# Kernel tuning notes

Hardware: AMD Instinct MI355X
Metric: run time of the kernel (lower is better)

The kernel has to match this reference:

```python
import jax, jax.numpy as jnp
import numpy as np


def setup_inputs() -> dict:
    key = jax.random.key(0)
    kq, kk, kv, km = jax.random.split(key, 4)
    B, H, S, D = 1, 16, 2048, 64
    q = jax.random.normal(kq, (B, H, S, D), dtype=jnp.float32)
    k = jax.random.normal(kk, (B, H, S, D), dtype=jnp.float32)
    v = jax.random.normal(kv, (B, H, S, D), dtype=jnp.float32)
    # Boolean attention mask: True = attend, False = ignore.
    # block-pruned use case while keeping the same dense-mask semantics.
    BLK = 64
    tile = jax.random.bernoulli(km, 0.5, (B, H, S // BLK, S // BLK))
    mask = jnp.repeat(jnp.repeat(tile, BLK, axis=2), BLK, axis=3)
    # Guarantee at least something per row is allowed in most rows is not
    # required: fully-masked rows legitimately produce zero output.
    return {"q": q, "k": k, "v": v, "mask": mask}


def reference(q, k, v, mask):
    # Masked scaled-dot-product attention; rows with no valid keys output 0,
    # matching the kernel's `acc / l_i if l_i > 0 else 0` behavior.
    D = q.shape[-1]
    scale = 1.0 / jnp.sqrt(jnp.asarray(D, q.dtype))
    qk = jnp.einsum("bhqd,bhkd->bhqk", q, k) * scale          # [B,H,S,S]
    neg_inf = jnp.asarray(-jnp.inf, qk.dtype)
    s = jnp.where(mask, qk, neg_inf)
    m = jnp.max(s, axis=-1, keepdims=True)                      # row max (may be -inf)
    m_safe = jnp.where(jnp.isfinite(m), m, jnp.zeros_like(m))
    p = jnp.where(mask, jnp.exp(s - m_safe), jnp.zeros_like(qk))  # unnormalized probs
    l = jnp.sum(p, axis=-1, keepdims=True)                      # [B,H,S,1]
    acc = jnp.einsum("bhqk,bhkd->bhqd", p, v)
    out = jnp.where(l > 0, acc / jnp.where(l > 0, l, jnp.ones_like(l)), jnp.zeros_like(acc))
    return out
```

## Files before the change

kernel.cpp:

```cpp
#include <hip/hip_runtime.h>
#include <hip/hip_bf16.h>
#include <stdint.h>

typedef __bf16 bf16;
typedef __attribute__((ext_vector_type(4))) __bf16 bf16x4;
typedef __attribute__((ext_vector_type(8))) __bf16 bf16x8;
typedef __attribute__((ext_vector_type(4))) float f32x4;
typedef __attribute__((ext_vector_type(4))) unsigned int u32x4;

#define NH 16
#define SEQ 2048
#define DH 64
#define NT 32
#define SCALE 0.125f
#define NEGINF (-1e30f)
#define IMG_TILE 8192

#define WS_KIMG  65536
#define WS_VIMG  (WS_KIMG + (size_t)NH * NT * IMG_TILE)
#define WS_NEED  (WS_VIMG + (size_t)NH * NT * IMG_TILE)

__device__ __forceinline__ unsigned swz16(int row, int bytecol) {
  return (unsigned)(row * 128 + (bytecol ^ ((row & 7) << 4)));
}

__global__ void __launch_bounds__(256) conv_kernel(
    const float* __restrict__ kg, const float* __restrict__ vg,
    unsigned char* __restrict__ ws)
{
  const int b = blockIdx.x, tid = threadIdx.x;
  const int h = b & 15, kt = (b >> 4) & 31, which = b >> 9;
  const int kb = kt << 6;
  __shared__ float T[64][65];
  const int row = tid >> 2, c0 = (tid & 3) * 16;

  const float* src = which ? vg : kg;
  {
    const f32x4* rp = (const f32x4*)(src + ((size_t)(h * SEQ) + kb + row) * DH + c0);
    f32x4 a0 = rp[0], a1 = rp[1], a2 = rp[2], a3 = rp[3];
    float* d = &T[row][c0];
    #pragma unroll
    for (int j = 0; j < 4; ++j) {
      d[j] = a0[j]; d[4 + j] = a1[j]; d[8 + j] = a2[j]; d[12 + j] = a3[j];
    }
  }
  __syncthreads();
  if (which == 0) {
    unsigned char* kimg = ws + WS_KIMG + (size_t)(h * NT + kt) * IMG_TILE;
    #pragma unroll
    for (int i = 0; i < 2; ++i) {
      const int slot = tid + 256 * i, g = slot >> 6, ll = slot & 63;
      const int nd = g >> 1, ks = g & 1;
      const float* s = &T[16 * nd + (ll & 15)][ks * 32 + (ll >> 4) * 8];
      bf16x8 o;
      #pragma unroll
      for (int j = 0; j < 8; ++j) o[j] = (bf16)s[j];
      *(bf16x8*)(kimg + slot * 16) = o;
    }
  } else {
    unsigned char* vimg = ws + WS_VIMG + (size_t)(h * NT + kt) * IMG_TILE;
    #pragma unroll
    for (int i = 0; i < 2; ++i) {
      const int slot = tid + 256 * i, g = slot >> 6, ll = slot & 63;
      const int nd = g >> 1, ks = g & 1;
      const int r0 = ks * 32 + (ll >> 4) * 8, col = 16 * nd + (ll & 15);
      bf16x8 o;
      #pragma unroll
      for (int j = 0; j < 8; ++j) o[j] = (bf16)T[r0 + j][col];
      *(bf16x8*)(vimg + slot * 16) = o;
    }
  }
}

template<bool IMG>
__global__ void __launch_bounds__(256, 4) fused_attn_kernel(
    const float* __restrict__ qg, const float* __restrict__ kg,
    const float* __restrict__ vg, const void* __restrict__ maskg,
    float* __restrict__ outg, const unsigned char* __restrict__ ws)
{
  const int bid = blockIdx.x;
  const int h = bid & 15, qt = bid >> 4, qb = qt << 6;
  const int tid = threadIdx.x, l = tid & 63, rw = tid >> 6;
  const int qrow = l & 15, kgrp = l >> 4;

  __shared__ __attribute__((aligned(16))) bf16 Pl[4][1024];
  __shared__ unsigned sOr[2][32], sAnd[2][32];
  __shared__ unsigned char tfl[32];
  __shared__ unsigned char Ll[32];
  __shared__ int lcnt;
  __shared__ int clsS;

  bf16x8 qa[2];
  {
    const float* qp = qg + ((size_t)(h * SEQ) + qb + 16 * rw + qrow) * DH;
    #pragma unroll
    for (int ks = 0; ks < 2; ++ks) {
      f32x4 x0 = *(const f32x4*)(qp + ks * 32 + kgrp * 8);
      f32x4 x1 = *(const f32x4*)(qp + ks * 32 + kgrp * 8 + 4);
      bf16x8 a;
      #pragma unroll
      for (int j = 0; j < 4; ++j) {
        a[j] = (bf16)(x0[j] * SCALE); a[4 + j] = (bf16)(x1[j] * SCALE);
      }
      qa[ks] = a;
    }
  }

  if (tid == 0) clsS = 0;
  __syncthreads();
  {
    u32x4 t = ((const u32x4*)maskg)[tid];
    int bits = 0;
    #pragma unroll
    for (int j = 0; j < 4; ++j) {
      if (t[j] == 0x01010101u) bits |= 1;
      else if (t[j] == 1u) bits |= 2;
    }
    const int wb = (__any(bits & 1) ? 1 : 0) | (__any(bits & 2) ? 2 : 0);
    if (l == 0 && wb) atomicOr(&clsS, wb);
  }
  __syncthreads();
  const int byteMode = ((clsS & 1) || !(clsS & 2)) ? 1 : 0;

  const int half = tid >> 7;
  if (byteMode) {
    const unsigned char* rp = (const unsigned char*)maskg
        + ((size_t)(h * SEQ) + qb + half * 63) * SEQ + (tid & 127) * 16;
    u32x4 t = *(const u32x4*)rp;
    unsigned o = t[0] | t[1] | t[2] | t[3];
    unsigned a = t[0] & t[1] & t[2] & t[3];
    o |= __shfl_xor(o, 1); a &= __shfl_xor(a, 1);
    o |= __shfl_xor(o, 2); a &= __shfl_xor(a, 2);
    if ((l & 3) == 0) {
      const int kt = ((tid >> 6) & 1) * 16 + (l >> 2);
      sOr[half][kt] = o; sAnd[half][kt] = a;
    }
  } else {
    const unsigned char* rbase = (const unsigned char*)maskg
        + ((size_t)(h * SEQ) + qb + half * 63) * (size_t)SEQ * 4;
    const int c0 = tid & 127;
    unsigned oo[4], aa[4];
    #pragma unroll
    for (int p = 0; p < 4; ++p) {
      u32x4 t = *(const u32x4*)(rbase + (p * 128 + c0) * 16);
      oo[p] = t[0] | t[1] | t[2] | t[3];
      aa[p] = t[0] & t[1] & t[2] & t[3];
    }
    #pragma unroll
    for (int d = 1; d <= 8; d <<= 1)
      #pragma unroll
      for (int p = 0; p < 4; ++p) {
        oo[p] |= __shfl_xor(oo[p], d); aa[p] &= __shfl_xor(aa[p], d);
      }
    if ((l & 15) == 0) {
      #pragma unroll
      for (int p = 0; p < 4; ++p) {
        const int kt = p * 8 + ((tid >> 6) & 1) * 4 + (l >> 4);
        sOr[half][kt] = oo[p]; sAnd[half][kt] = aa[p];
      }
    }
  }
  __syncthreads();
  if (tid < 32) {
    const int kt = tid;
    const unsigned o0 = sOr[0][kt], a0 = sAnd[0][kt];
    const unsigned o1 = sOr[1][kt], a1 = sAnd[1][kt];
    int active, allT = 0;
    if (o0 == a0 && o1 == a1 && o0 == o1) {
      if (o0 == 0u) active = 0;
      else {
        active = 1;
        allT = byteMode
             ? (((((a0 & 0x7F7F7F7Fu) + 0x7F7F7F7Fu) | a0) & 0x80808080u) == 0x80808080u)
             : 1;
      }
    } else {
      active = ((o0 | o1) != 0u);
    }
    tfl[kt] = (unsigned char)(active | (allT ? 2 : 0));
  }
  __syncthreads();
  if (tid == 0) {
    int n = 0;
    for (int kt = 0; kt < NT; ++kt) {
      const unsigned f = tfl[kt];
      if (f & 1) Ll[n++] = (unsigned char)(kt | ((f & 2) ? 0x80 : 0));
    }
    lcnt = n;
  }
  __syncthreads();
  const int cnt = lcnt;

  f32x4 oacc[4];
  #pragma unroll
  for (int nd = 0; nd < 4; ++nd) oacc[nd] = (f32x4){0.f, 0.f, 0.f, 0.f};
  float mrun = NEGINF, lrun = 0.f;

  auto loadK = [&](bf16x8 (&kf)[8], int kt) {
    if constexpr (IMG) {
      const unsigned char* kp = ws + WS_KIMG + (size_t)(h * NT + kt) * IMG_TILE + l * 16;
      #pragma unroll
      for (int g = 0; g < 8; ++g) kf[g] = *(const bf16x8*)(kp + g * 1024);
    } else {
      const int kb = kt << 6;
      #pragma unroll
      for (int g = 0; g < 8; ++g) {
        const int nd = g >> 1, ks = g & 1;
        const float* kr = kg + ((size_t)(h * SEQ) + kb + 16 * nd + qrow) * DH
                          + ks * 32 + kgrp * 8;
        f32x4 x0 = ((const f32x4*)kr)[0], x1 = ((const f32x4*)kr)[1];
        #pragma unroll
        for (int j = 0; j < 4; ++j) { kf[g][j] = (bf16)x0[j]; kf[g][4 + j] = (bf16)x1[j]; }
      }
    }
  };

  bf16x8 kf[8];
  if (cnt > 0) loadK(kf, Ll[0] & 63);

  char* pw = (char*)Pl[rw];

  for (int i = 0; i < cnt; ++i) {
    const unsigned e = Ll[i];
    const int kt = e & 63;
    const int allT = (e & 0x80u) != 0;
    const int kb = kt << 6;

    f32x4 sfr[4];
    #pragma unroll
    for (int nd = 0; nd < 4; ++nd) sfr[nd] = (f32x4){0.f, 0.f, 0.f, 0.f};
    __builtin_amdgcn_s_setprio(1);
    #pragma unroll
    for (int nd = 0; nd < 4; ++nd)
      #pragma unroll
      for (int ks = 0; ks < 2; ++ks)
        sfr[nd] = __builtin_amdgcn_mfma_f32_16x16x32_bf16(kf[nd * 2 + ks], qa[ks], sfr[nd], 0, 0, 0);
    __builtin_amdgcn_s_setprio(0);

    if (i + 1 < cnt) loadK(kf, Ll[i + 1] & 63);

    bf16x8 vf[8];
    if constexpr (IMG) {
      const unsigned char* vp = ws + WS_VIMG + (size_t)(h * NT + kt) * IMG_TILE + l * 16;
      #pragma unroll
      for (int g = 0; g < 8; ++g) vf[g] = *(const bf16x8*)(vp + g * 1024);
    } else {
      #pragma unroll
      for (int g = 0; g < 8; ++g) {
        const int nd = g >> 1, ks = g & 1;
        const float* vb = vg + ((size_t)(h * SEQ) + kb + ks * 32 + kgrp * 8) * DH
                          + 16 * nd + qrow;
        #pragma unroll
        for (int j = 0; j < 8; ++j) vf[g][j] = (bf16)vb[j * DH];
      }
    }

    if (!allT) {
      const size_t base = ((size_t)(h * SEQ) + qb + 16 * rw + qrow) * SEQ + kb + 4 * kgrp;
      #pragma unroll
      for (int nd = 0; nd < 4; ++nd)
        #pragma unroll
        for (int r = 0; r < 4; ++r) {
          const size_t off = base + 16 * nd + r;
          const bool mv = byteMode ? (((const unsigned char*)maskg)[off] != 0)
                                   : (((const unsigned*)maskg)[off] != 0u);
          if (!mv) sfr[nd][r] = NEGINF;
        }
    }

    float mt;
    {
      f32x4 t0, t1;
      #pragma unroll
      for (int r = 0; r < 4; ++r) {
        t0[r] = fmaxf(sfr[0][r], sfr[1][r]);
        t1[r] = fmaxf(sfr[2][r], sfr[3][r]);
      }
      mt = fmaxf(fmaxf(fmaxf(t0[0], t0[1]), fmaxf(t0[2], t0[3])),
                 fmaxf(fmaxf(t1[0], t1[1]), fmaxf(t1[2], t1[3])));
    }
    mt = fmaxf(mt, __shfl_xor(mt, 16));
    mt = fmaxf(mt, __shfl_xor(mt, 32));
    const float mn = fmaxf(mrun, mt);
    const float fac = __expf(mrun - mn);
    float ls = 0.f;
    bf16x4 pb[4];
    #pragma unroll
    for (int nd = 0; nd < 4; ++nd)
      #pragma unroll
      for (int r = 0; r < 4; ++r) {
        const float p = (sfr[nd][r] > -1e20f) ? __expf(sfr[nd][r] - mn) : 0.f;
        ls += p; pb[nd][r] = (bf16)p;
      }
    ls += __shfl_xor(ls, 16);
    ls += __shfl_xor(ls, 32);
    lrun = lrun * fac + ls;
    mrun = mn;
    #pragma unroll
    for (int nd = 0; nd < 4; ++nd)
      #pragma unroll
      for (int r = 0; r < 4; ++r) oacc[nd][r] *= fac;

    #pragma unroll
    for (int nd = 0; nd < 4; ++nd)
      *(bf16x4*)(pw + swz16(qrow, 32 * nd + 8 * kgrp)) = pb[nd];
    bf16x8 ap[2];
    #pragma unroll
    for (int ks = 0; ks < 2; ++ks)
      ap[ks] = *(const bf16x8*)(pw + swz16(qrow, 64 * ks + 16 * kgrp));

    __builtin_amdgcn_s_setprio(1);
    #pragma unroll
    for (int ks = 0; ks < 2; ++ks)
      #pragma unroll
      for (int nd = 0; nd < 4; ++nd)
        oacc[nd] = __builtin_amdgcn_mfma_f32_16x16x32_bf16(vf[nd * 2 + ks], ap[ks], oacc[nd], 0, 0, 0);
    __builtin_amdgcn_s_setprio(0);
  }

  {
    const float inv = (lrun > 0.f) ? (1.f / lrun) : 0.f;
    const int grow = qb + 16 * rw + qrow;
    float* op = outg + ((size_t)(h * SEQ) + grow) * DH + 4 * kgrp;
    #pragma unroll
    for (int nd = 0; nd < 4; ++nd) {
      f32x4 o;
      #pragma unroll
      for (int r = 0; r < 4; ++r) o[r] = oacc[nd][r] * inv;
      *(f32x4*)(op + 16 * nd) = o;
    }
  }
}

extern "C" void kernel_launch(void* const* d_in, const int* in_sizes, int n_in,
                              void* d_out, int out_size, void* d_ws, size_t ws_size,
                              hipStream_t stream) {
  const float* q = (const float*)d_in[0];
  const float* k = (const float*)d_in[1];
  const float* v = (const float*)d_in[2];
  const void*  m = d_in[3];
  float* out = (float*)d_out;
  unsigned char* ws = (unsigned char*)d_ws;

  if (ws_size >= WS_NEED) {
    conv_kernel<<<2 * NH * NT, 256, 0, stream>>>(k, v, ws);
    fused_attn_kernel<true><<<NH * NT, 256, 0, stream>>>(q, k, v, m, out, ws);
  } else {
    fused_attn_kernel<false><<<NH * NT, 256, 0, stream>>>(q, k, v, m, out, ws);
  }
}
```

Measured before the change: 40.10 us.

## Split key tiles across two wave groups per block and merge softmax state

Doubles the block to 512 threads so two groups of four waves each take alternate active key tiles for the same 64 query rows. At the end, the second group writes its running max, running sum and output accumulator to shared memory, and the first group rescales and combines both before writing the output. The aim is to halve the serial per-block loop over key tiles and raise the number of waves in flight per CU. The cost is more shared memory, an extra combine step with two block barriers, and higher register pressure under the new launch bounds.

```diff
diff --git a/kernel.cpp b/kernel.cpp
--- a/kernel.cpp
+++ b/kernel.cpp
@@ -73,17 +73,19 @@
 }
 
 template<bool IMG>
-__global__ void __launch_bounds__(256, 4) fused_attn_kernel(
+__global__ void __launch_bounds__(512, 4) fused_attn_kernel(
     const float* __restrict__ qg, const float* __restrict__ kg,
     const float* __restrict__ vg, const void* __restrict__ maskg,
     float* __restrict__ outg, const unsigned char* __restrict__ ws)
 {
   const int bid = blockIdx.x;
   const int h = bid & 15, qt = bid >> 4, qb = qt << 6;
-  const int tid = threadIdx.x, l = tid & 63, rw = tid >> 6;
+  const int tid = threadIdx.x, l = tid & 63, w = tid >> 6;
+  const int s = w >> 2, rw = w & 3;
   const int qrow = l & 15, kgrp = l >> 4;
 
-  __shared__ __attribute__((aligned(16))) bf16 Pl[4][1024];
+  __shared__ __attribute__((aligned(16))) bf16 Pl[8][1024];
+  __shared__ float mg[4][64][19];
   __shared__ unsigned sOr[2][32], sAnd[2][32];
   __shared__ unsigned char tfl[32];
   __shared__ unsigned char Ll[32];
@@ -122,41 +124,43 @@
   __syncthreads();
   const int byteMode = ((clsS & 1) || !(clsS & 2)) ? 1 : 0;
 
-  const int half = tid >> 7;
-  if (byteMode) {
-    const unsigned char* rp = (const unsigned char*)maskg
-        + ((size_t)(h * SEQ) + qb + half * 63) * SEQ + (tid & 127) * 16;
-    u32x4 t = *(const u32x4*)rp;
-    unsigned o = t[0] | t[1] | t[2] | t[3];
-    unsigned a = t[0] & t[1] & t[2] & t[3];
-    o |= __shfl_xor(o, 1); a &= __shfl_xor(a, 1);
-    o |= __shfl_xor(o, 2); a &= __shfl_xor(a, 2);
-    if ((l & 3) == 0) {
-      const int kt = ((tid >> 6) & 1) * 16 + (l >> 2);
-      sOr[half][kt] = o; sAnd[half][kt] = a;
-    }
-  } else {
-    const unsigned char* rbase = (const unsigned char*)maskg
-        + ((size_t)(h * SEQ) + qb + half * 63) * (size_t)SEQ * 4;
-    const int c0 = tid & 127;
-    unsigned oo[4], aa[4];
-    #pragma unroll
-    for (int p = 0; p < 4; ++p) {
-      u32x4 t = *(const u32x4*)(rbase + (p * 128 + c0) * 16);
-      oo[p] = t[0] | t[1] | t[2] | t[3];
-      aa[p] = t[0] & t[1] & t[2] & t[3];
-    }
-    #pragma unroll
-    for (int d = 1; d <= 8; d <<= 1)
+  if (tid < 256) {
+    const int half = tid >> 7;
+    if (byteMode) {
+      const unsigned char* rp = (const unsigned char*)maskg
+          + ((size_t)(h * SEQ) + qb + half * 63) * SEQ + (tid & 127) * 16;
+      u32x4 t = *(const u32x4*)rp;
+      unsigned o = t[0] | t[1] | t[2] | t[3];
+      unsigned a = t[0] & t[1] & t[2] & t[3];
+      o |= __shfl_xor(o, 1); a &= __shfl_xor(a, 1);
+      o |= __shfl_xor(o, 2); a &= __shfl_xor(a, 2);
+      if ((l & 3) == 0) {
+        const int kt = ((tid >> 6) & 1) * 16 + (l >> 2);
+        sOr[half][kt] = o; sAnd[half][kt] = a;
+      }
+    } else {
+      const unsigned char* rbase = (const unsigned char*)maskg
+          + ((size_t)(h * SEQ) + qb + half * 63) * (size_t)SEQ * 4;
+      const int c0 = tid & 127;
+      unsigned oo[4], aa[4];
       #pragma unroll
       for (int p = 0; p < 4; ++p) {
-        oo[p] |= __shfl_xor(oo[p], d); aa[p] &= __shfl_xor(aa[p], d);
-      }
-    if ((l & 15) == 0) {
-      #pragma unroll
-      for (int p = 0; p < 4; ++p) {
-        const int kt = p * 8 + ((tid >> 6) & 1) * 4 + (l >> 4);
-        sOr[half][kt] = oo[p]; sAnd[half][kt] = aa[p];
+        u32x4 t = *(const u32x4*)(rbase + (p * 128 + c0) * 16);
+        oo[p] = t[0] | t[1] | t[2] | t[3];
+        aa[p] = t[0] & t[1] & t[2] & t[3];
+      }
+      #pragma unroll
+      for (int d = 1; d <= 8; d <<= 1)
+        #pragma unroll
+        for (int p = 0; p < 4; ++p) {
+          oo[p] |= __shfl_xor(oo[p], d); aa[p] &= __shfl_xor(aa[p], d);
+        }
+      if ((l & 15) == 0) {
+        #pragma unroll
+        for (int p = 0; p < 4; ++p) {
+          const int kt = p * 8 + ((tid >> 6) & 1) * 4 + (l >> 4);
+          sOr[half][kt] = oo[p]; sAnd[half][kt] = aa[p];
+        }
       }
     }
   }
@@ -216,11 +220,11 @@
   };
 
   bf16x8 kf[8];
-  if (cnt > 0) loadK(kf, Ll[0] & 63);
-
-  char* pw = (char*)Pl[rw];
-
-  for (int i = 0; i < cnt; ++i) {
+  if (s < cnt) loadK(kf, Ll[s] & 63);
+
+  char* pw = (char*)Pl[w];
+
+  for (int i = s; i < cnt; i += 2) {
     const unsigned e = Ll[i];
     const int kt = e & 63;
     const int allT = (e & 0x80u) != 0;
@@ -237,7 +241,7 @@
         sfr[nd] = __builtin_amdgcn_mfma_f32_16x16x32_bf16(kf[nd * 2 + ks], qa[ks], sfr[nd], 0, 0, 0);
     __builtin_amdgcn_s_setprio(0);
 
-    if (i + 1 < cnt) loadK(kf, Ll[i + 1] & 63);
+    if (i + 2 < cnt) loadK(kf, Ll[i + 2] & 63);
 
     bf16x8 vf[8];
     if constexpr (IMG) {
@@ -318,15 +322,31 @@
     __builtin_amdgcn_s_setprio(0);
   }
 
-  {
-    const float inv = (lrun > 0.f) ? (1.f / lrun) : 0.f;
+  __syncthreads();
+  if (s == 1) {
+    float* mp = &mg[rw][l][0];
+    mp[0] = mrun; mp[1] = lrun;
+    #pragma unroll
+    for (int nd = 0; nd < 4; ++nd)
+      #pragma unroll
+      for (int r = 0; r < 4; ++r) mp[2 + nd * 4 + r] = oacc[nd][r];
+  }
+  __syncthreads();
+  if (s == 0) {
+    const float* mp = &mg[rw][l][0];
+    const float m1 = mp[0], l1 = mp[1];
+    const float ms = fmaxf(mrun, m1);
+    const float f0 = __expf(mrun - ms), f1 = __expf(m1 - ms);
+    const float li = lrun * f0 + l1 * f1;
+    const float inv = (li > 0.f) ? (1.f / li) : 0.f;
     const int grow = qb + 16 * rw + qrow;
     float* op = outg + ((size_t)(h * SEQ) + grow) * DH + 4 * kgrp;
     #pragma unroll
     for (int nd = 0; nd < 4; ++nd) {
       f32x4 o;
       #pragma unroll
-      for (int r = 0; r < 4; ++r) o[r] = oacc[nd][r] * inv;
+      for (int r = 0; r < 4; ++r)
+        o[r] = (oacc[nd][r] * f0 + mp[2 + nd * 4 + r] * f1) * inv;
       *(f32x4*)(op + 16 * nd) = o;
     }
   }
@@ -344,8 +364,8 @@
 
   if (ws_size >= WS_NEED) {
     conv_kernel<<<2 * NH * NT, 256, 0, stream>>>(k, v, ws);
-    fused_attn_kernel<true><<<NH * NT, 256, 0, stream>>>(q, k, v, m, out, ws);
+    fused_attn_kernel<true><<<NH * NT, 512, 0, stream>>>(q, k, v, m, out, ws);
   } else {
-    fused_attn_kernel<false><<<NH * NT, 256, 0, stream>>>(q, k, v, m, out, ws);
+    fused_attn_kernel<false><<<NH * NT, 512, 0, stream>>>(q, k, v, m, out, ws);
   }
 }
```

New measurement: 42.26 us. +5.4%, slower.

## Skip online-softmax rescale when max grows little and defer row-sum reduction

Applied to the files above, without the earlier changes.

Adds a lazy rescaling rule to the attention loop. The running max and the accumulator rescale are updated only when some lane's tile max exceeds the running max by more than 8, with the exponent threshold checked wave-wide. The per-tile cross-lane shuffles for the row sum are replaced by per-lane partial sums that are reduced once after the loop, and tiles with an all-true mask skip the -inf test on each element. The tile list entry is also made wave-uniform with readfirstlane. In exchange, probabilities can reach up to e^8 before normalization, which costs some precision headroom in bf16 and fp32, and the skip test adds a wave vote on each iteration.

```diff
diff --git a/kernel.cpp b/kernel.cpp
--- a/kernel.cpp
+++ b/kernel.cpp
@@ -194,7 +194,8 @@
   f32x4 oacc[4];
   #pragma unroll
   for (int nd = 0; nd < 4; ++nd) oacc[nd] = (f32x4){0.f, 0.f, 0.f, 0.f};
-  float mrun = NEGINF, lrun = 0.f;
+  float mrun = NEGINF;
+  float lrun = 0.f;
 
   auto loadK = [&](bf16x8 (&kf)[8], int kt) {
     if constexpr (IMG) {
@@ -216,14 +217,14 @@
   };
 
   bf16x8 kf[8];
-  if (cnt > 0) loadK(kf, Ll[0] & 63);
+  if (cnt > 0) loadK(kf, __builtin_amdgcn_readfirstlane((int)Ll[0]) & 63);
 
   char* pw = (char*)Pl[rw];
 
   for (int i = 0; i < cnt; ++i) {
-    const unsigned e = Ll[i];
+    const int e = __builtin_amdgcn_readfirstlane((int)Ll[i]);
     const int kt = e & 63;
-    const int allT = (e & 0x80u) != 0;
+    const int allT = (e & 0x80) != 0;
     const int kb = kt << 6;
 
     f32x4 sfr[4];
@@ -237,7 +238,7 @@
         sfr[nd] = __builtin_amdgcn_mfma_f32_16x16x32_bf16(kf[nd * 2 + ks], qa[ks], sfr[nd], 0, 0, 0);
     __builtin_amdgcn_s_setprio(0);
 
-    if (i + 1 < cnt) loadK(kf, Ll[i + 1] & 63);
+    if (i + 1 < cnt) loadK(kf, __builtin_amdgcn_readfirstlane((int)Ll[i + 1]) & 63);
 
     bf16x8 vf[8];
     if constexpr (IMG) {
@@ -268,7 +269,7 @@
         }
     }
 
-    float mt;
+    float pmax;
     {
       f32x4 t0, t1;
       #pragma unroll
@@ -276,30 +277,42 @@
         t0[r] = fmaxf(sfr[0][r], sfr[1][r]);
         t1[r] = fmaxf(sfr[2][r], sfr[3][r]);
       }
-      mt = fmaxf(fmaxf(fmaxf(t0[0], t0[1]), fmaxf(t0[2], t0[3])),
-                 fmaxf(fmaxf(t1[0], t1[1]), fmaxf(t1[2], t1[3])));
-    }
-    mt = fmaxf(mt, __shfl_xor(mt, 16));
-    mt = fmaxf(mt, __shfl_xor(mt, 32));
-    const float mn = fmaxf(mrun, mt);
-    const float fac = __expf(mrun - mn);
+      pmax = fmaxf(fmaxf(fmaxf(t0[0], t0[1]), fmaxf(t0[2], t0[3])),
+                   fmaxf(fmaxf(t1[0], t1[1]), fmaxf(t1[2], t1[3])));
+    }
+    if (!__all(pmax - mrun <= 8.f)) {
+      float mt = pmax;
+      mt = fmaxf(mt, __shfl_xor(mt, 16));
+      mt = fmaxf(mt, __shfl_xor(mt, 32));
+      const float mn = fmaxf(mrun, mt);
+      const float fac = __expf(mrun - mn);
+      lrun *= fac;
+      #pragma unroll
+      for (int nd = 0; nd < 4; ++nd)
+        #pragma unroll
+        for (int r = 0; r < 4; ++r) oacc[nd][r] *= fac;
+      mrun = mn;
+    }
     float ls = 0.f;
     bf16x4 pb[4];
-    #pragma unroll
-    for (int nd = 0; nd < 4; ++nd)
-      #pragma unroll
-      for (int r = 0; r < 4; ++r) {
-        const float p = (sfr[nd][r] > -1e20f) ? __expf(sfr[nd][r] - mn) : 0.f;
-        ls += p; pb[nd][r] = (bf16)p;
-      }
-    ls += __shfl_xor(ls, 16);
-    ls += __shfl_xor(ls, 32);
-    lrun = lrun * fac + ls;
-    mrun = mn;
-    #pragma unroll
-    for (int nd = 0; nd < 4; ++nd)
-      #pragma unroll
-      for (int r = 0; r < 4; ++r) oacc[nd][r] *= fac;
+    if (allT) {
+      #pragma unroll
+      for (int nd = 0; nd < 4; ++nd)
+        #pragma unroll
+        for (int r = 0; r < 4; ++r) {
+          const float p = __expf(sfr[nd][r] - mrun);
+          ls += p; pb[nd][r] = (bf16)p;
+        }
+    } else {
+      #pragma unroll
+      for (int nd = 0; nd < 4; ++nd)
+        #pragma unroll
+        for (int r = 0; r < 4; ++r) {
+          const float p = (sfr[nd][r] > -1e20f) ? __expf(sfr[nd][r] - mrun) : 0.f;
+          ls += p; pb[nd][r] = (bf16)p;
+        }
+    }
+    lrun += ls;
 
     #pragma unroll
     for (int nd = 0; nd < 4; ++nd)
@@ -317,6 +330,9 @@
         oacc[nd] = __builtin_amdgcn_mfma_f32_16x16x32_bf16(vf[nd * 2 + ks], ap[ks], oacc[nd], 0, 0, 0);
     __builtin_amdgcn_s_setprio(0);
   }
+
+  lrun += __shfl_xor(lrun, 16);
+  lrun += __shfl_xor(lrun, 32);
 
   {
     const float inv = (lrun > 0.f) ? (1.f / lrun) : 0.f;
```

Measured after the change: 83.26 us. +107.6%, slower.
